# Kernel optimization log

Measured on AMD Instinct MI355X. Metric: run time of the kernel, lower is better.

## Reference

```python
import jax, jax.numpy as jnp
import numpy as np

BOX = 100.0      # points live in [0, BOX)^3
STRIDE = 128     # > BOX/voxel_size, used for linearizing 3D voxel coords


def setup_inputs() -> dict:
    key = jax.random.key(0)
    k1, k2 = jax.random.split(key)
    N, C = 2_000_000, 32
    positions = jax.random.uniform(k1, (N, 3), dtype=jnp.float32) * BOX
    features = jax.random.normal(k2, (N, C), dtype=jnp.float32)
    voxel_size = jnp.ones((), dtype=jnp.float32)
    return {"positions": positions, "features": features, "voxel_size": voxel_size}


def reference(positions, features, voxel_size):
    """VoxelPooling(position_fn='center', feature_fn='max').

    Output is padded to N rows (M <= N real voxels); `valid` marks real voxels.
    Voxel grid is aligned to the origin; pooled position is the voxel center.
    """
    N = positions.shape[0]
    # integer voxel coordinates (positions are non-negative here)
    coords = jnp.floor(positions / voxel_size).astype(jnp.int32)           # [N,3]
    lin = coords[:, 0] + STRIDE * coords[:, 1] + STRIDE * STRIDE * coords[:, 2]  # [N]
    # compact unique voxels; jit-compatible with fixed size=N, pad with -1
    uniq, inv = jnp.unique(lin, size=N, fill_value=-1, return_inverse=True)
    # per-voxel max over features (empty segments get dtype-min, masked below)
    pooled_features = jax.ops.segment_max(features, inv, num_segments=N)   # [N,C]
    # decode voxel coords from linear key -> voxel centers
    cz = uniq // (STRIDE * STRIDE)
    rem = uniq % (STRIDE * STRIDE)
    cy = rem // STRIDE
    cx = rem % STRIDE
    centers = (jnp.stack([cx, cy, cz], axis=-1).astype(positions.dtype) + 0.5) * voxel_size
    valid = uniq >= 0                                                      # [N]
    pooled_positions = jnp.where(valid[:, None], centers, 0.0)
    pooled_features = jnp.where(valid[:, None], pooled_features, 0.0)
    return pooled_positions, pooled_features, valid
```

## Files before the change

kernel.cpp:

```cpp
#include <hip/hip_runtime.h>
#include <stdint.h>

#define STRIDE 128
#define NVOX (STRIDE * STRIDE * STRIDE)
#define BINVOX 512
#define NBIN (NVOX / BINVOX)
#define HB 256
#define HT 1024
#define NSEG 16
#define SEGBINS (NBIN / NSEG)
#define CAP 1536
#define LINCAP 8192

typedef unsigned long long u64;

__device__ __forceinline__ uint32_t enc_f32(float f) {
  uint32_t u = __float_as_uint(f);
  return (u & 0x80000000u) ? ~u : (u | 0x80000000u);
}
__device__ __forceinline__ float dec_f32(uint32_t e) {
  uint32_t u = (e & 0x80000000u) ? (e & 0x7fffffffu) : ~e;
  return __uint_as_float(u);
}

__device__ __forceinline__ uint32_t cnt_eq1(uint32_t w) {
  uint32_t y = w ^ 0x01010101u;
  uint32_t z = ~(((y & 0x7F7F7F7Fu) + 0x7F7F7F7Fu) | y | 0x7F7F7F7Fu);
  return __popc(z);
}

__device__ __forceinline__ uint32_t src_of(uint32_t u, const uint32_t* csum,
                                           const uint32_t* offs) {
  uint32_t lo = 0, hi = HB - 1;
  #pragma unroll
  for (int it = 0; it < 8; ++it) {
    uint32_t mid = (lo + hi) >> 1;
    bool gt = csum[mid] > u;
    hi = gt ? mid : hi;
    lo = gt ? lo : mid + 1;
  }
  uint32_t prev = lo ? csum[lo - 1] : 0u;
  return offs[lo] + (u - prev);
}

__global__ __launch_bounds__(HT) void k_build(
    const float* __restrict__ pos, const float* __restrict__ vs_p,
    uint8_t* __restrict__ bytemap, uint32_t* __restrict__ loff,
    uint32_t* __restrict__ pairs, uint32_t* __restrict__ sync,
    float* __restrict__ out_pos, float* __restrict__ out_feat,
    float* __restrict__ out_valid, int n, int vbound, int srow) {
  __shared__ uint32_t h[NBIN];
  __shared__ uint32_t wsum[HT / 64];
  __shared__ uint32_t linbuf[LINCAP];
  int t = threadIdx.x;

  if (blockIdx.x >= HB) {
    size_t gid = (size_t)(blockIdx.x - HB) * HT + t;
    int row = vbound + (int)(gid >> 3);
    int q = (int)(gid & 7);
    if (row >= n) return;
    if (row < srow)
      ((float4*)out_feat)[(size_t)row * 8 + q] = make_float4(0.f, 0.f, 0.f, 0.f);
    if (q == 0) {
      out_pos[(size_t)row * 3 + 0] = 0.f;
      out_pos[(size_t)row * 3 + 1] = 0.f;
      out_pos[(size_t)row * 3 + 2] = 0.f;
      out_valid[row] = 0.f;
    }
    return;
  }

  int b = blockIdx.x;
  if (b == 0 && t == 0) *sync = 0u;
  for (int k = t; k < NBIN; k += HT) h[k] = 0u;
  __syncthreads();
  int chunk = (n + HB - 1) / HB;
  int i0 = b * chunk, i1 = min(n, i0 + chunk);
  int len = i1 - i0;
  float vs = vs_p[0];
  for (int j = t; j < len; j += HT) {
    size_t i = (size_t)(i0 + j);
    float x = pos[3 * i + 0];
    float y = pos[3 * i + 1];
    float z = pos[3 * i + 2];
    int lin = (int)floorf(x / vs) + STRIDE * (int)floorf(y / vs) +
              STRIDE * STRIDE * (int)floorf(z / vs);
    linbuf[j] = (uint32_t)lin;
    bytemap[lin] = 1;
    atomicAdd(&h[lin >> 9], 1u);
  }
  __syncthreads();
  uint32_t v0 = h[t * 4 + 0], v1 = h[t * 4 + 1], v2 = h[t * 4 + 2], v3 = h[t * 4 + 3];
  uint32_t s3 = v0 + v1 + v2 + v3;
  uint32_t inc = s3;
  #pragma unroll
  for (int d = 1; d < 64; d <<= 1) {
    uint32_t o = __shfl_up(inc, d, 64);
    if ((t & 63) >= d) inc += o;
  }
  if ((t & 63) == 63) wsum[t >> 6] = inc;
  __syncthreads();
  if (t < 16) {
    uint32_t wv = wsum[t], wi = wv;
    #pragma unroll
    for (int d = 1; d < 16; d <<= 1) {
      uint32_t o = __shfl_up(wi, d, 16);
      if (t >= d) wi += o;
    }
    wsum[t] = wi - wv;
  }
  __syncthreads();
  uint32_t run = wsum[t >> 6] + (inc - s3);
  uint32_t* lr = &loff[(size_t)b * NBIN + t * 4];
  uint32_t c0 = run; lr[0] = run; run += v0;
  uint32_t c1 = run; lr[1] = run; run += v1;
  uint32_t c2 = run; lr[2] = run; run += v2;
  uint32_t c3 = run; lr[3] = run;
  __syncthreads();
  h[t * 4 + 0] = (uint32_t)i0 + c0;
  h[t * 4 + 1] = (uint32_t)i0 + c1;
  h[t * 4 + 2] = (uint32_t)i0 + c2;
  h[t * 4 + 3] = (uint32_t)i0 + c3;
  __syncthreads();
  for (int j = t; j < len; j += HT) {
    int lin = (int)linbuf[j];
    uint32_t slot = atomicAdd(&h[lin >> 9], 1u);
    pairs[slot] = ((uint32_t)(lin & (BINVOX - 1)) << 21) | (uint32_t)(i0 + j);
  }
}

__global__ __launch_bounds__(SEGBINS) void k_scan(
    const uint32_t* __restrict__ bytemap_w, uint32_t* __restrict__ occ_base,
    uint32_t* __restrict__ sync, uint32_t* __restrict__ seg_tot,
    uint32_t* __restrict__ Mp) {
  __shared__ uint32_t s[SEGBINS];
  int b = blockIdx.x, t = threadIdx.x;
  int bin = b * SEGBINS + t;
  const uint4* bp = (const uint4*)bytemap_w + (size_t)bin * 32;
  uint32_t occ = 0;
  #pragma unroll
  for (int k = 0; k < 32; ++k) {
    uint4 v = bp[k];
    occ += cnt_eq1(v.x) + cnt_eq1(v.y) + cnt_eq1(v.z) + cnt_eq1(v.w);
  }
  s[t] = occ;
  __syncthreads();
  for (int off = 1; off < SEGBINS; off <<= 1) {
    uint32_t a = (t >= off) ? s[t - off] : 0u;
    __syncthreads();
    s[t] += a;
    __syncthreads();
  }
  uint32_t excl = s[t] - occ;
  if (t == 0) {
    __hip_atomic_store(&seg_tot[b], s[SEGBINS - 1], __ATOMIC_RELEASE,
                       __HIP_MEMORY_SCOPE_AGENT);
    __hip_atomic_fetch_add(sync, 1u, __ATOMIC_ACQ_REL, __HIP_MEMORY_SCOPE_AGENT);
    while (__hip_atomic_load(sync, __ATOMIC_ACQUIRE, __HIP_MEMORY_SCOPE_AGENT) <
           (uint32_t)NSEG) {}
  }
  __syncthreads();
  uint32_t pre = 0, grand = 0;
  #pragma unroll
  for (int i = 0; i < NSEG; ++i) {
    uint32_t v = __hip_atomic_load(&seg_tot[i], __ATOMIC_ACQUIRE,
                                   __HIP_MEMORY_SCOPE_AGENT);
    if (i < b) pre += v;
    grand += v;
  }
  occ_base[bin] = pre + excl;
  if (b == 0 && t == 0) Mp[0] = grand;
}

__global__ __launch_bounds__(HT) void k_pool(
    const float* __restrict__ feat, const float* __restrict__ vs_p,
    const uint32_t* __restrict__ pairs, const uint32_t* __restrict__ loff,
    const uint32_t* __restrict__ occ_base, const uint8_t* __restrict__ bytemap,
    const uint32_t* __restrict__ Mp,
    float* __restrict__ out_pos, float* __restrict__ out_feat,
    float* __restrict__ out_valid, int n, int vbound) {
  __shared__ uint32_t smax[BINVOX * 32];
  __shared__ u64 sbw[8];
  __shared__ uint32_t offs[HB], csum[HB];
  __shared__ uint32_t srcidx[CAP];
  int t = threadIdx.x;

  if (blockIdx.x >= NBIN) {
    size_t gid = (size_t)(blockIdx.x - NBIN) * HT + t;
    int row = (int)(gid >> 3);
    int q = (int)(gid & 7);
    if (row >= vbound) return;
    uint32_t M = Mp[0];
    if ((uint32_t)row < M) return;
    ((float4*)out_feat)[(size_t)row * 8 + q] = make_float4(0.f, 0.f, 0.f, 0.f);
    if (q == 0) {
      out_pos[(size_t)row * 3 + 0] = 0.f;
      out_pos[(size_t)row * 3 + 1] = 0.f;
      out_pos[(size_t)row * 3 + 2] = 0.f;
      out_valid[row] = 0.f;
    }
    return;
  }

  int bin = blockIdx.x;
  #pragma unroll
  for (int k = 0; k < 16; ++k) smax[t + k * HT] = 0u;
  if (t < 512) {
    uint32_t occb = bytemap[(size_t)bin * BINVOX + t];
    u64 m = __ballot(occb == 1u);
    if ((t & 63) == 0) sbw[t >> 6] = m;
  }
  int chunk = (n + HB - 1) / HB;
  if (t < HB) {
    int i0b = t * chunk, i1b = min(n, i0b + chunk);
    uint32_t lo = loff[(size_t)t * NBIN + bin];
    uint32_t hi = (bin == NBIN - 1) ? (uint32_t)(i1b - i0b)
                                    : loff[(size_t)t * NBIN + bin + 1];
    offs[t] = (uint32_t)i0b + lo;
    csum[t] = hi - lo;
  }
  __syncthreads();
  if (t < 64) {
    uint32_t c0 = csum[t * 4], c1 = csum[t * 4 + 1];
    uint32_t c2 = csum[t * 4 + 2], c3 = csum[t * 4 + 3];
    uint32_t s1 = c0 + c1, s2 = s1 + c2, s3 = s2 + c3;
    uint32_t inc = s3;
    #pragma unroll
    for (int d = 1; d < 64; d <<= 1) {
      uint32_t o = __shfl_up(inc, d, 64);
      if (t >= d) inc += o;
    }
    uint32_t base = inc - s3;
    csum[t * 4]     = base + c0;
    csum[t * 4 + 1] = base + s1;
    csum[t * 4 + 2] = base + s2;
    csum[t * 4 + 3] = base + s3;
  }
  __syncthreads();
  uint32_t cnt = csum[HB - 1];
  if (cnt == 0) return;

  bool fits = (cnt <= (uint32_t)CAP);
  if (fits) {
    if (t < HB) {
      uint32_t beg = t ? csum[t - 1] : 0u;
      uint32_t len = csum[t] - beg;
      uint32_t o = offs[t];
      for (uint32_t j = 0; j < len; ++j) srcidx[beg + j] = o + j;
    }
    __syncthreads();
  }

  int g = t >> 5;
  int ch = t & 31;
  uint32_t last = cnt - 1;
  for (uint32_t u = (uint32_t)g; u < cnt; u += 256) {
    uint32_t pp[8];
    #pragma unroll
    for (int k = 0; k < 8; ++k) {
      uint32_t uu = min(u + 32u * k, last);
      uint32_t s = fits ? srcidx[uu] : src_of(uu, csum, offs);
      pp[k] = pairs[s];
    }
    float vv[8];
    #pragma unroll
    for (int k = 0; k < 8; ++k)
      vv[k] = feat[(size_t)(pp[k] & 0x1FFFFFu) * 32 + ch];
    #pragma unroll
    for (int k = 0; k < 8; ++k)
      atomicMax(&smax[(pp[k] >> 21) * 32 + ch], enc_f32(vv[k]));
  }
  __syncthreads();

  int vb = t >> 1, half = t & 1;
  u64 w = sbw[vb >> 6];
  int bit = vb & 63;
  if ((w >> bit) & 1ull) {
    uint32_t lr = (uint32_t)__popcll(w & ((1ull << bit) - 1ull));
    for (int ww = 0; ww < (vb >> 6); ++ww) lr += (uint32_t)__popcll(sbw[ww]);
    uint32_t rank = occ_base[bin] + lr;
    float4* orow = (float4*)(out_feat + (size_t)rank * 32 + half * 16);
    #pragma unroll
    for (int j = 0; j < 4; ++j) {
      const uint32_t* sp = &smax[vb * 32 + half * 16 + j * 4];
      float4 o;
      o.x = dec_f32(sp[0]); o.y = dec_f32(sp[1]);
      o.z = dec_f32(sp[2]); o.w = dec_f32(sp[3]);
      orow[j] = o;
    }
    if (half == 0) {
      float vs = vs_p[0];
      int lin = bin * BINVOX + vb;
      int cx = lin & 127, cy = (lin >> 7) & 127, cz = lin >> 14;
      out_pos[(size_t)rank * 3 + 0] = ((float)cx + 0.5f) * vs;
      out_pos[(size_t)rank * 3 + 1] = ((float)cy + 0.5f) * vs;
      out_pos[(size_t)rank * 3 + 2] = ((float)cz + 0.5f) * vs;
      out_valid[rank] = 1.0f;
    }
  }
}

__global__ void k_tail2(float4* __restrict__ dst, long long cnt4) {
  long long i = (long long)blockIdx.x * blockDim.x + threadIdx.x;
  if (i < cnt4) dst[i] = make_float4(0.f, 0.f, 0.f, 0.f);
}

extern "C" void kernel_launch(void* const* d_in, const int* in_sizes, int n_in,
                              void* d_out, int out_size, void* d_ws, size_t ws_size,
                              hipStream_t stream) {
  const float* pos  = (const float*)d_in[0];
  const float* feat = (const float*)d_in[1];
  const float* vs   = (const float*)d_in[2];
  int n = in_sizes[0] / 3;

  float*    out_pos   = (float*)d_out;
  uint32_t* out_feat  = (uint32_t*)(out_pos + (size_t)n * 3);
  float*    out_valid = (float*)((float*)out_feat + (size_t)n * 32);

  int vbound = n < 1000000 ? n : 1000000;

  size_t scratch_u32 = (size_t)n + (size_t)HB * NBIN + NBIN + NVOX / 4;
  size_t ws_need = 256 + scratch_u32 * 4;

  uint32_t* Mp      = (uint32_t*)d_ws;
  uint32_t* sync    = Mp + 1;
  uint32_t* seg_tot = Mp + 8;

  uint32_t* base;
  int srow;
  if (ws_size >= ws_need) {
    base = (uint32_t*)((char*)d_ws + 256);
    srow = n;
  } else {
    base = out_feat + (size_t)n * 32 - scratch_u32;
    srow = (int)(((size_t)n * 32 - scratch_u32) / 32);
  }
  uint32_t* pairs    = base;
  uint32_t* loff     = pairs + n;
  uint32_t* occ_base = loff + (size_t)HB * NBIN;
  uint8_t*  bytemap  = (uint8_t*)(occ_base + NBIN);

  int hard_blocks = (int)(((size_t)(n - vbound) * 8 + HT - 1) / HT);
  k_build<<<HB + hard_blocks, HT, 0, stream>>>(
      pos, vs, bytemap, loff, pairs, sync, out_pos, (float*)out_feat,
      out_valid, n, vbound, srow);
  k_scan<<<NSEG, SEGBINS, 0, stream>>>((const uint32_t*)bytemap, occ_base,
                                       sync, seg_tot, Mp);
  int soft_blocks = (int)(((size_t)vbound * 8 + HT - 1) / HT);
  k_pool<<<NBIN + soft_blocks, HT, 0, stream>>>(
      feat, vs, pairs, loff, occ_base, bytemap, Mp,
      out_pos, (float*)out_feat, out_valid, n, vbound);
  if (srow < n) {
    long long cnt4 = ((long long)n * 32 - (long long)srow * 32) / 4;
    k_tail2<<<(int)((cnt4 + 1023) / 1024), 1024, 0, stream>>>(
        (float4*)(out_feat + (size_t)srow * 32), cnt4);
  }
}
```

Before: 200.5 us.

## Vectorize feature gather to float4, swizzle shared max slots, use nontemporal zero stores

Result: faster. 192.9 us (-3.8%).

```diff
diff --git a/kernel.cpp b/kernel.cpp
--- a/kernel.cpp
+++ b/kernel.cpp
@@ -13,6 +13,7 @@
 #define LINCAP 8192
 
 typedef unsigned long long u64;
+typedef float nfloat4 __attribute__((ext_vector_type(4)));
 
 __device__ __forceinline__ uint32_t enc_f32(float f) {
   uint32_t u = __float_as_uint(f);
@@ -41,6 +42,11 @@
   }
   uint32_t prev = lo ? csum[lo - 1] : 0u;
   return offs[lo] + (u - prev);
+}
+
+__device__ __forceinline__ void nt_zero4(void* p) {
+  nfloat4 z = {0.f, 0.f, 0.f, 0.f};
+  __builtin_nontemporal_store(z, (nfloat4*)p);
 }
 
 __global__ __launch_bounds__(HT) void k_build(
@@ -60,7 +66,7 @@
     int q = (int)(gid & 7);
     if (row >= n) return;
     if (row < srow)
-      ((float4*)out_feat)[(size_t)row * 8 + q] = make_float4(0.f, 0.f, 0.f, 0.f);
+      nt_zero4(((float4*)out_feat) + (size_t)row * 8 + q);
     if (q == 0) {
       out_pos[(size_t)row * 3 + 0] = 0.f;
       out_pos[(size_t)row * 3 + 1] = 0.f;
@@ -192,7 +198,7 @@
     if (row >= vbound) return;
     uint32_t M = Mp[0];
     if ((uint32_t)row < M) return;
-    ((float4*)out_feat)[(size_t)row * 8 + q] = make_float4(0.f, 0.f, 0.f, 0.f);
+    nt_zero4(((float4*)out_feat) + (size_t)row * 8 + q);
     if (q == 0) {
       out_pos[(size_t)row * 3 + 0] = 0.f;
       out_pos[(size_t)row * 3 + 1] = 0.f;
@@ -251,24 +257,32 @@
     __syncthreads();
   }
 
-  int g = t >> 5;
-  int ch = t & 31;
+  int g = t >> 3;
+  int q = t & 7;
+  const float4* f4 = (const float4*)feat;
   uint32_t last = cnt - 1;
-  for (uint32_t u = (uint32_t)g; u < cnt; u += 256) {
+  for (uint32_t u = (uint32_t)g; u < cnt; u += 1024) {
     uint32_t pp[8];
     #pragma unroll
     for (int k = 0; k < 8; ++k) {
-      uint32_t uu = min(u + 32u * k, last);
+      uint32_t uu = min(u + 128u * k, last);
       uint32_t s = fits ? srcidx[uu] : src_of(uu, csum, offs);
       pp[k] = pairs[s];
     }
-    float vv[8];
+    float4 vv[8];
     #pragma unroll
     for (int k = 0; k < 8; ++k)
-      vv[k] = feat[(size_t)(pp[k] & 0x1FFFFFu) * 32 + ch];
-    #pragma unroll
-    for (int k = 0; k < 8; ++k)
-      atomicMax(&smax[(pp[k] >> 21) * 32 + ch], enc_f32(vv[k]));
+      vv[k] = f4[(size_t)(pp[k] & 0x1FFFFFu) * 8 + q];
+    #pragma unroll
+    for (int k = 0; k < 8; ++k) {
+      uint32_t vb = pp[k] >> 21;
+      uint32_t* sb = &smax[vb * 32];
+      uint32_t c = (uint32_t)q * 4 + vb;
+      atomicMax(&sb[(c + 0) & 31], enc_f32(vv[k].x));
+      atomicMax(&sb[(c + 1) & 31], enc_f32(vv[k].y));
+      atomicMax(&sb[(c + 2) & 31], enc_f32(vv[k].z));
+      atomicMax(&sb[(c + 3) & 31], enc_f32(vv[k].w));
+    }
   }
   __syncthreads();
 
@@ -280,12 +294,15 @@
     for (int ww = 0; ww < (vb >> 6); ++ww) lr += (uint32_t)__popcll(sbw[ww]);
     uint32_t rank = occ_base[bin] + lr;
     float4* orow = (float4*)(out_feat + (size_t)rank * 32 + half * 16);
+    const uint32_t* sb = &smax[vb * 32];
     #pragma unroll
     for (int j = 0; j < 4; ++j) {
-      const uint32_t* sp = &smax[vb * 32 + half * 16 + j * 4];
+      uint32_t c = (uint32_t)half * 16 + j * 4 + vb;
       float4 o;
-      o.x = dec_f32(sp[0]); o.y = dec_f32(sp[1]);
-      o.z = dec_f32(sp[2]); o.w = dec_f32(sp[3]);
+      o.x = dec_f32(sb[(c + 0) & 31]);
+      o.y = dec_f32(sb[(c + 1) & 31]);
+      o.z = dec_f32(sb[(c + 2) & 31]);
+      o.w = dec_f32(sb[(c + 3) & 31]);
       orow[j] = o;
     }
     if (half == 0) {
@@ -302,7 +319,7 @@
 
 __global__ void k_tail2(float4* __restrict__ dst, long long cnt4) {
   long long i = (long long)blockIdx.x * blockDim.x + threadIdx.x;
-  if (i < cnt4) dst[i] = make_float4(0.f, 0.f, 0.f, 0.f);
+  if (i < cnt4) nt_zero4(dst + i);
 }
 
 extern "C" void kernel_launch(void* const* d_in, const int* in_sizes, int n_in,
```
